# Kernel optimization log

Hardware: AMD Instinct MI355X
Metric: run time of the kernel (lower is better)

Reference implementation:

```python
import jax, jax.numpy as jnp
import numpy as np

D_MODEL = 1024
N_HEADS = 16
D_K = D_MODEL // N_HEADS
B, T = 4, 2048


def setup_inputs() -> dict:
    key = jax.random.key(0)
    ks = jax.random.split(key, 12)
    s = 1.0 / np.sqrt(D_MODEL)
    inp = {
        "query": jax.random.normal(ks[0], (B, T, D_MODEL), dtype=jnp.float32),
        "key": jax.random.normal(ks[1], (B, T, D_MODEL), dtype=jnp.float32),
        "value": jax.random.normal(ks[2], (B, T, D_MODEL), dtype=jnp.float32),
        # causal mask, broadcastable over batch and heads
        "mask": jnp.tril(jnp.ones((T, T), dtype=bool))[None, None, :, :],
        "W_q": jax.random.uniform(ks[3], (D_MODEL, D_MODEL), jnp.float32, -s, s),
        "b_q": jnp.zeros((D_MODEL,), jnp.float32),
        "W_k": jax.random.uniform(ks[4], (D_MODEL, D_MODEL), jnp.float32, -s, s),
        "b_k": jnp.zeros((D_MODEL,), jnp.float32),
        "W_v": jax.random.uniform(ks[5], (D_MODEL, D_MODEL), jnp.float32, -s, s),
        "b_v": jnp.zeros((D_MODEL,), jnp.float32),
        "W_o": jax.random.uniform(ks[6], (D_MODEL, D_MODEL), jnp.float32, -s, s),
        "b_o": jnp.zeros((D_MODEL,), jnp.float32),
    }
    return inp


def _split_heads(x):
    b, t, _ = x.shape
    return x.reshape(b, t, N_HEADS, D_K).transpose(0, 2, 1, 3)  # [B,H,T,Dk]


def reference(query, key, value, mask, W_q, b_q, W_k, b_k, W_v, b_v, W_o, b_o):
    q = _split_heads(query @ W_q.T + b_q)
    k = _split_heads(key @ W_k.T + b_k)
    v = _split_heads(value @ W_v.T + b_v)
    scale = 1.0 / jnp.sqrt(jnp.asarray(D_K, q.dtype))
    scores = jnp.einsum("bhqd,bhkd->bhqk", q, k) * scale  # [B,H,Tq,Tk]
    scores = jnp.where(mask, scores, jnp.asarray(-jnp.inf, scores.dtype))
    attn = jax.nn.softmax(scores, axis=-1)
    out = jnp.einsum("bhqk,bhkd->bhqd", attn, v)
    out = out.transpose(0, 2, 1, 3).reshape(query.shape[0], query.shape[1], D_MODEL)
    return out @ W_o.T + b_o
```

## Files before the change

### kernel.cpp

```cpp
#include <hip/hip_runtime.h>
#include <stdint.h>
#include <stddef.h>


typedef __attribute__((ext_vector_type(4))) float f32x4;
typedef __attribute__((ext_vector_type(8))) _Float16 f16x8;
typedef __attribute__((ext_vector_type(4))) _Float16 f16x4;

#define DEV __device__ __forceinline__

constexpr int BATCH = 4, SEQ = 2048, NH = 16, DK = 64, DM = 1024;
constexpr int MROWS = BATCH * SEQ;
constexpr float QSCALE = 0.125f * 1.4426950408889634f;

DEV void async16(const void* g, void* l) {
  __builtin_amdgcn_global_load_lds(
      (const __attribute__((address_space(1))) unsigned int*)g,
      (__attribute__((address_space(3))) unsigned int*)l, 16, 0, 0);
}

__global__ void cvt_w_kernel(const float* __restrict__ w0, const float* __restrict__ w1,
                             const float* __restrict__ w2, const float* __restrict__ w3,
                             _Float16* __restrict__ o0, _Float16* __restrict__ o1,
                             _Float16* __restrict__ o2, _Float16* __restrict__ o3) {
  size_t i = (size_t)blockIdx.x * blockDim.x + threadIdx.x;
  const float* ws[4] = {w0, w1, w2, w3};
  _Float16* os[4] = {o0, o1, o2, o3};
#pragma unroll
  for (int m = 0; m < 4; m++) {
    f32x4 x = *(const f32x4*)(ws[m] + i * 4);
    f16x4 h;
#pragma unroll
    for (int j = 0; j < 4; j++) h[j] = (_Float16)x[j];
    *(f16x4*)(os[m] + i * 4) = h;
  }
}

__global__ void cvt_act_kernel(const float* __restrict__ a0, const float* __restrict__ a1,
                               const float* __restrict__ a2, _Float16* __restrict__ o0,
                               _Float16* __restrict__ o1, _Float16* __restrict__ o2) {
  size_t i = (size_t)blockIdx.x * blockDim.x + threadIdx.x;
  const float* as[3] = {a0, a1, a2};
  _Float16* os[3] = {o0, o1, o2};
#pragma unroll
  for (int m = 0; m < 3; m++) {
    f32x4 x = *(const f32x4*)(as[m] + i * 4);
    f16x4 h;
#pragma unroll
    for (int j = 0; j < 4; j++) h[j] = (_Float16)x[j];
    *(f16x4*)(os[m] + i * 4) = h;
  }
}

struct QKVPtrs {
  const float* a32[3];
  const _Float16* a16[3];
  const _Float16* w[3];
  const float* bias[3];
  _Float16* out[3];
};

DEV void stage_g16(const _Float16* __restrict__ src, int k0, _Float16* dst, int tid) {
  const int wave = tid >> 6;
#pragma unroll
  for (int it = 0; it < 4; it++) {
    int idx = it * 256 + tid;
    int row = idx >> 3, seg = idx & 7;
    async16(src + (size_t)row * DM + k0 + ((seg ^ (row & 7)) << 3),
            (char*)dst + (size_t)(it * 256 + wave * 64) * 16);
  }
}

DEV void stage_f32(const float* __restrict__ src, int k0, _Float16* dst, int tid) {
#pragma unroll
  for (int it = 0; it < 4; it++) {
    int idx = it * 256 + tid;
    int row = idx >> 3, seg = idx & 7;
    const float* g = src + (size_t)row * DM + k0 + seg * 8;
    f32x4 x0 = *(const f32x4*)g;
    f32x4 x1 = *(const f32x4*)(g + 4);
    f16x8 h;
#pragma unroll
    for (int j = 0; j < 4; j++) { h[j] = (_Float16)x0[j]; h[4 + j] = (_Float16)x1[j]; }
    *(f16x8*)&dst[row * 64 + ((seg ^ (row & 7)) << 3)] = h;
  }
}

template <bool AH>
__global__ __launch_bounds__(256) void gemm_qkv_kernel(QKVPtrs P) {
  constexpr int K = DM;
  __shared__ __align__(16) _Float16 smem[4 * 128 * 64];
  const int z = blockIdx.z;
  const _Float16* Bw = P.w[z];
  const int tid = threadIdx.x;
  const int wave = tid >> 6, lane = tid & 63;
  const int quad = lane >> 4, l16 = lane & 15;
  const int wm = wave >> 1, wn = wave & 1;
  const int m0 = blockIdx.x * 128, n0 = blockIdx.y * 128;
  const float scale = (z == 0) ? QSCALE : 1.0f;

  const _Float16* Bg = Bw + (size_t)n0 * K;
  const _Float16* Ag16 = AH ? P.a16[z] + (size_t)m0 * K : nullptr;
  const float* Ag32 = AH ? nullptr : P.a32[z] + (size_t)m0 * K;

  const f32x4 zero4 = {0.f, 0.f, 0.f, 0.f};
  f32x4 acc[4][4];
#pragma unroll
  for (int mt = 0; mt < 4; mt++)
#pragma unroll
    for (int nt = 0; nt < 4; nt++) acc[mt][nt] = zero4;

  float bv[4];
#pragma unroll
  for (int nt = 0; nt < 4; nt++) bv[nt] = P.bias[z][n0 + wn * 64 + nt * 16 + l16];

  stage_g16(Bg, 0, smem + 8192, tid);
  if (AH) stage_g16(Ag16, 0, smem, tid);
  else    stage_f32(Ag32, 0, smem, tid);
  __syncthreads();

  for (int kt = 0; kt < K / 64; kt++) {
    const int boff = (kt & 1) ? 16384 : 0;
    const _Float16* Asc = smem + boff;
    const _Float16* Bsc = smem + 8192 + boff;
    if (kt + 1 < K / 64) {
      const int k0 = (kt + 1) * 64;
      const int poff = boff ^ 16384;
      stage_g16(Bg, k0, smem + 8192 + poff, tid);
      if (AH) stage_g16(Ag16, k0, smem + poff, tid);
      else    stage_f32(Ag32, k0, smem + poff, tid);
    }
    __builtin_amdgcn_s_setprio(1);
#pragma unroll
    for (int ks = 0; ks < 2; ks++) {
      f16x8 af[4], bfr[4];
#pragma unroll
      for (int mt = 0; mt < 4; mt++) {
        int r = wm * 64 + mt * 16 + l16;
        af[mt] = *(const f16x8*)&Asc[r * 64 + (((ks * 4 + quad) ^ (r & 7)) << 3)];
      }
#pragma unroll
      for (int nt = 0; nt < 4; nt++) {
        int r = wn * 64 + nt * 16 + l16;
        bfr[nt] = *(const f16x8*)&Bsc[r * 64 + (((ks * 4 + quad) ^ (r & 7)) << 3)];
      }
#pragma unroll
      for (int mt = 0; mt < 4; mt++)
#pragma unroll
        for (int nt = 0; nt < 4; nt++)
          acc[mt][nt] = __builtin_amdgcn_mfma_f32_16x16x32_f16(af[mt], bfr[nt], acc[mt][nt], 0, 0, 0);
    }
    __builtin_amdgcn_s_setprio(0);
    __syncthreads();
  }

  _Float16* Ct = smem;
  const int b = m0 >> 11, tbase = m0 & (SEQ - 1);
  if (z < 2) {
#pragma unroll
    for (int mt = 0; mt < 4; mt++)
#pragma unroll
      for (int nt = 0; nt < 4; nt++)
#pragma unroll
        for (int i = 0; i < 4; i++)
          Ct[(wm * 64 + mt * 16 + quad * 4 + i) * 144 + wn * 64 + nt * 16 + l16] =
              (_Float16)((acc[mt][nt][i] + bv[nt]) * scale);
  } else {
#pragma unroll
    for (int mt = 0; mt < 4; mt++)
#pragma unroll
      for (int nt = 0; nt < 4; nt++)
#pragma unroll
        for (int i = 0; i < 4; i++)
          Ct[(wn * 64 + nt * 16 + l16) * 144 + wm * 64 + mt * 16 + quad * 4 + i] =
              (_Float16)(acc[mt][nt][i] + bv[nt]);
  }
  __syncthreads();
  _Float16* out = P.out[z];
  if (z < 2) {
    const int row = tid >> 1, coff = (tid & 1) * 32;
#pragma unroll
    for (int hh = 0; hh < 2; hh++) {
      int h = (n0 >> 6) + hh;
      size_t gb = ((size_t)(b * NH + h) * SEQ + tbase) * 64 + (size_t)tid * 32;
#pragma unroll
      for (int k2 = 0; k2 < 4; k2++)
        *(f16x8*)&out[gb + k2 * 8] =
            *(const f16x8*)&Ct[row * 144 + hh * 64 + coff + k2 * 8];
    }
  } else {
#pragma unroll
    for (int k2 = 0; k2 < 8; k2++) {
      int c = k2 * 256 + tid;
      int n = c >> 4, s2 = c & 15;
      int h = (n0 + n) >> 6, d = (n0 + n) & (DK - 1);
      size_t gb = ((size_t)(b * NH + h) * DK + d) * SEQ + tbase + s2 * 8;
      *(f16x8*)&out[gb] = *(const f16x8*)&Ct[n * 144 + s2 * 8];
    }
  }
}

__global__ __launch_bounds__(256) void gemm_out_kernel(
    const _Float16* __restrict__ Ah, const _Float16* __restrict__ Bw,
    const float* __restrict__ bias, float* __restrict__ Cp) {
  constexpr int K = DM;
  __shared__ __align__(16) _Float16 smem[4 * 128 * 64];
  const int tid = threadIdx.x;
  const int wave = tid >> 6, lane = tid & 63;
  const int quad = lane >> 4, l16 = lane & 15;
  const int wm = wave >> 1, wn = wave & 1;
  const int m0 = blockIdx.x * 128, n0 = blockIdx.y * 128;

  const _Float16* Bg = Bw + (size_t)n0 * K;
  const _Float16* Ag = Ah + (size_t)m0 * K;

  const f32x4 zero4 = {0.f, 0.f, 0.f, 0.f};
  f32x4 acc[4][4];
#pragma unroll
  for (int mt = 0; mt < 4; mt++)
#pragma unroll
    for (int nt = 0; nt < 4; nt++) acc[mt][nt] = zero4;

  float bv[4];
#pragma unroll
  for (int nt = 0; nt < 4; nt++) bv[nt] = bias[n0 + wn * 64 + nt * 16 + l16];

  stage_g16(Bg, 0, smem + 8192, tid);
  stage_g16(Ag, 0, smem, tid);
  __syncthreads();

  for (int kt = 0; kt < K / 64; kt++) {
    const int boff = (kt & 1) ? 16384 : 0;
    const _Float16* Asc = smem + boff;
    const _Float16* Bsc = smem + 8192 + boff;
    if (kt + 1 < K / 64) {
      const int k0 = (kt + 1) * 64;
      const int poff = boff ^ 16384;
      stage_g16(Bg, k0, smem + 8192 + poff, tid);
      stage_g16(Ag, k0, smem + poff, tid);
    }
    __builtin_amdgcn_s_setprio(1);
#pragma unroll
    for (int ks = 0; ks < 2; ks++) {
      f16x8 af[4], bfr[4];
#pragma unroll
      for (int mt = 0; mt < 4; mt++) {
        int r = wm * 64 + mt * 16 + l16;
        af[mt] = *(const f16x8*)&Asc[r * 64 + (((ks * 4 + quad) ^ (r & 7)) << 3)];
      }
#pragma unroll
      for (int nt = 0; nt < 4; nt++) {
        int r = wn * 64 + nt * 16 + l16;
        bfr[nt] = *(const f16x8*)&Bsc[r * 64 + (((ks * 4 + quad) ^ (r & 7)) << 3)];
      }
#pragma unroll
      for (int mt = 0; mt < 4; mt++)
#pragma unroll
        for (int nt = 0; nt < 4; nt++)
          acc[mt][nt] = __builtin_amdgcn_mfma_f32_16x16x32_f16(af[mt], bfr[nt], acc[mt][nt], 0, 0, 0);
    }
    __builtin_amdgcn_s_setprio(0);
    __syncthreads();
  }
#pragma unroll
  for (int mt = 0; mt < 4; mt++)
#pragma unroll
    for (int nt = 0; nt < 4; nt++)
#pragma unroll
      for (int i = 0; i < 4; i++) {
        int m = m0 + wm * 64 + mt * 16 + quad * 4 + i;
        int n = n0 + wn * 64 + nt * 16 + l16;
        Cp[(size_t)m * DM + n] = acc[mt][nt][i] + bv[nt];
      }
}

__global__ __launch_bounds__(256, 2) void attn_kernel(
    const _Float16* __restrict__ Q, const _Float16* __restrict__ Kt,
    const _Float16* __restrict__ V, _Float16* __restrict__ O) {
  __shared__ __align__(16) _Float16 Ks[128 * 72];
  __shared__ __align__(16) _Float16 Vs[64 * 136];
  const int tid = threadIdx.x;
  const int wave = tid >> 6, lane = tid & 63, quad = lane >> 4, l16 = lane & 15;
  const int bh = blockIdx.y;
  const size_t base = (size_t)bh * SEQ * DK;
  const int b = bh >> 4, h = bh & 15;
  const f32x4 zero4 = {0.f, 0.f, 0.f, 0.f};

  for (int p = 0; p < 2; p++) {
    const int qt = (p == 0) ? (int)blockIdx.x : 15 - (int)blockIdx.x;
    const int t0 = qt * 128;

    f16x8 qf[2][2];
#pragma unroll
    for (int mt = 0; mt < 2; mt++)
#pragma unroll
      for (int ks = 0; ks < 2; ks++)
        qf[mt][ks] = *(const f16x8*)(Q + base + (size_t)(t0 + wave * 32 + mt * 16 + l16) * DK +
                                     ks * 32 + quad * 8);

    f32x4 oacc[2][4];
#pragma unroll
    for (int mt = 0; mt < 2; mt++)
#pragma unroll
      for (int nt = 0; nt < 4; nt++) oacc[mt][nt] = zero4;
    float mrow[2] = {-1e30f, -1e30f}, lrow[2] = {0.f, 0.f};

    for (int j = 0; j <= qt; j++) {
#pragma unroll
      for (int it = 0; it < 4; it++) {
        int c = it * 256 + tid;
        int row = c >> 3, off = (c & 7) * 8;
        *(f16x8*)&Ks[row * 72 + off] =
            *(const f16x8*)(Kt + base + (size_t)(j * 128 + row) * 64 + off);
      }
#pragma unroll
      for (int it = 0; it < 4; it++) {
        int c = it * 256 + tid;
        int d = c >> 4, off = (c & 15) * 8;
        *(f16x8*)&Vs[d * 136 + off] =
            *(const f16x8*)(V + base + ((size_t)d << 11) + j * 128 + off);
      }
      __syncthreads();

      f32x4 s[2][8];
#pragma unroll
      for (int nt = 0; nt < 8; nt++) {
        f16x8 kf0 = *(const f16x8*)&Ks[(nt * 16 + l16) * 72 + quad * 8];
        f16x8 kf1 = *(const f16x8*)&Ks[(nt * 16 + l16) * 72 + 32 + quad * 8];
#pragma unroll
        for (int mt = 0; mt < 2; mt++) {
          f32x4 zz = zero4;
          zz = __builtin_amdgcn_mfma_f32_16x16x32_f16(kf0, qf[mt][0], zz, 0, 0, 0);
          zz = __builtin_amdgcn_mfma_f32_16x16x32_f16(kf1, qf[mt][1], zz, 0, 0, 0);
          s[mt][nt] = zz;
        }
      }
      if (j == qt) {
#pragma unroll
        for (int mt = 0; mt < 2; mt++) {
          int qloc = wave * 32 + mt * 16 + l16;
#pragma unroll
          for (int nt = 0; nt < 8; nt++)
#pragma unroll
            for (int i = 0; i < 4; i++)
              if (nt * 16 + quad * 4 + i > qloc) s[mt][nt][i] = -1e30f;
        }
      }
#pragma unroll
      for (int mt = 0; mt < 2; mt++) {
        float mx = mrow[mt];
#pragma unroll
        for (int nt = 0; nt < 8; nt++)
#pragma unroll
          for (int i = 0; i < 4; i++) mx = fmaxf(mx, s[mt][nt][i]);
        mx = fmaxf(mx, __shfl_xor(mx, 16));
        mx = fmaxf(mx, __shfl_xor(mx, 32));
        float alpha = __builtin_exp2f(mrow[mt] - mx);
        mrow[mt] = mx;
        float rs = 0.f;
#pragma unroll
        for (int nt = 0; nt < 8; nt++)
#pragma unroll
          for (int i = 0; i < 4; i++) {
            float pv = __builtin_exp2f(s[mt][nt][i] - mx);
            s[mt][nt][i] = pv;
            rs += pv;
          }
        rs += __shfl_xor(rs, 16);
        rs += __shfl_xor(rs, 32);
        lrow[mt] = lrow[mt] * alpha + rs;
#pragma unroll
        for (int i = 0; i < 4; i++) {
          float ab = __shfl(alpha, quad * 4 + i);
#pragma unroll
          for (int nt = 0; nt < 4; nt++) oacc[mt][nt][i] *= ab;
        }
      }
#pragma unroll
      for (int jj = 0; jj < 8; jj++) {
        f16x4 pf[2];
#pragma unroll
        for (int mt = 0; mt < 2; mt++) {
          f16x4 t;
#pragma unroll
          for (int i = 0; i < 4; i++) t[i] = (_Float16)s[mt][jj][i];
          pf[mt] = t;
        }
#pragma unroll
        for (int nt = 0; nt < 4; nt++) {
          f16x4 vb = *(const f16x4*)&Vs[(nt * 16 + l16) * 136 + jj * 16 + quad * 4];
#pragma unroll
          for (int mt = 0; mt < 2; mt++)
            oacc[mt][nt] = __builtin_amdgcn_mfma_f32_16x16x16f16(pf[mt], vb, oacc[mt][nt], 0, 0, 0);
        }
      }
      __syncthreads();
    }
#pragma unroll
    for (int mt = 0; mt < 2; mt++) {
      float linv = 1.0f / lrow[mt];
#pragma unroll
      for (int i = 0; i < 4; i++) {
        float lb = __shfl(linv, quad * 4 + i);
        int t = t0 + wave * 32 + mt * 16 + quad * 4 + i;
#pragma unroll
        for (int nt = 0; nt < 4; nt++) {
          int d = nt * 16 + l16;
          O[((size_t)(b * SEQ + t) << 10) + h * 64 + d] = (_Float16)(oacc[mt][nt][i] * lb);
        }
      }
    }
  }
}

extern "C" void kernel_launch(void* const* d_in, const int* in_sizes, int n_in,
                              void* d_out, int out_size, void* d_ws, size_t ws_size,
                              hipStream_t stream) {
  const float* query = (const float*)d_in[0];
  const float* key_  = (const float*)d_in[1];
  const float* value = (const float*)d_in[2];
  const float* W_q = (const float*)d_in[4];
  const float* b_q = (const float*)d_in[5];
  const float* W_k = (const float*)d_in[6];
  const float* b_k = (const float*)d_in[7];
  const float* W_v = (const float*)d_in[8];
  const float* b_v = (const float*)d_in[9];
  const float* W_o = (const float*)d_in[10];
  const float* b_o = (const float*)d_in[11];

  constexpr size_t WEL = (size_t)DM * DM;
  constexpr size_t MEL = (size_t)MROWS * DM;
  _Float16* ws = (_Float16*)d_ws;
  _Float16* wq = ws;
  _Float16* wk = wq + WEL;
  _Float16* wv = wk + WEL;
  _Float16* wo = wv + WEL;

  const bool big = ws_size >= (size_t)(4 * WEL + 6 * MEL) * sizeof(_Float16);

  QKVPtrs P;
  P.a32[0] = query; P.a32[1] = key_; P.a32[2] = value;
  P.w[0] = wq; P.w[1] = wk; P.w[2] = wv;
  P.bias[0] = b_q; P.bias[1] = b_k; P.bias[2] = b_v;

  cvt_w_kernel<<<dim3((unsigned)(WEL / 4 / 256)), 256, 0, stream>>>(
      W_q, W_k, W_v, W_o, wq, wk, wv, wo);

  _Float16 *qb, *kb, *vb, *ab;
  if (big) {
    _Float16* qh = wo + WEL;
    _Float16* kh = qh + MEL;
    _Float16* vh = kh + MEL;
    qb = vh + MEL; kb = qb + MEL; vb = kb + MEL;
    ab = qh;
    P.a16[0] = qh; P.a16[1] = kh; P.a16[2] = vh;
    P.out[0] = qb; P.out[1] = kb; P.out[2] = vb;
    cvt_act_kernel<<<dim3((unsigned)(MEL / 4 / 256)), 256, 0, stream>>>(
        query, key_, value, qh, kh, vh);
    gemm_qkv_kernel<true><<<dim3(MROWS / 128, DM / 128, 3), 256, 0, stream>>>(P);
  } else {
    qb = wo + WEL; kb = qb + MEL; vb = kb + MEL; ab = vb + MEL;
    P.a16[0] = P.a16[1] = P.a16[2] = nullptr;
    P.out[0] = qb; P.out[1] = kb; P.out[2] = vb;
    gemm_qkv_kernel<false><<<dim3(MROWS / 128, DM / 128, 3), 256, 0, stream>>>(P);
  }

  attn_kernel<<<dim3(8, BATCH * NH), 256, 0, stream>>>(qb, kb, vb, ab);

  gemm_out_kernel<<<dim3(MROWS / 128, DM / 128), 256, 0, stream>>>(ab, wo, b_o, (float*)d_out);
}
```

Before: 329.7 us.

## Double-buffer K/V tiles in attention with async global-to-LDS loads and XOR swizzle

Replaces the synchronous register-staged K/V tile loads in the attention loop with async global_load_lds into two LDS buffers, prefetching tile j+1 while tile j is computed. Padded LDS rows are replaced by an XOR-swizzled layout to avoid bank conflicts without padding, and MFMA sections are wrapped in s_setprio raises. The aim is to hide global load latency behind compute. LDS usage roughly doubles, which may affect the two-blocks-per-CU occupancy. A single __syncthreads per iteration is relied on for ordering between the async writes and the reads.

New measurement: 335.4 us. Within noise of the previous version (+1.7%).

```diff
diff --git a/kernel.cpp b/kernel.cpp
--- a/kernel.cpp
+++ b/kernel.cpp
@@ -277,8 +277,8 @@
 __global__ __launch_bounds__(256, 2) void attn_kernel(
     const _Float16* __restrict__ Q, const _Float16* __restrict__ Kt,
     const _Float16* __restrict__ V, _Float16* __restrict__ O) {
-  __shared__ __align__(16) _Float16 Ks[128 * 72];
-  __shared__ __align__(16) _Float16 Vs[64 * 136];
+  __shared__ __align__(16) _Float16 Ks[2 * 128 * 64];
+  __shared__ __align__(16) _Float16 Vs[2 * 64 * 128];
   const int tid = threadIdx.x;
   const int wave = tid >> 6, lane = tid & 63, quad = lane >> 4, l16 = lane & 15;
   const int bh = blockIdx.y;
@@ -286,6 +286,13 @@
   const int b = bh >> 4, h = bh & 15;
   const f32x4 zero4 = {0.f, 0.f, 0.f, 0.f};
 
+  int koffs[2], voffs[8];
+#pragma unroll
+  for (int ks = 0; ks < 2; ks++) koffs[ks] = ((ks * 4 + quad) ^ (l16 & 7)) << 3;
+#pragma unroll
+  for (int jj = 0; jj < 8; jj++)
+    voffs[jj] = (((jj * 2 + (quad >> 1)) ^ l16) << 3) + (quad & 1) * 4;
+
   for (int p = 0; p < 2; p++) {
     const int qt = (p == 0) ? (int)blockIdx.x : 15 - (int)blockIdx.x;
     const int t0 = qt * 128;
@@ -305,28 +312,56 @@
       for (int nt = 0; nt < 4; nt++) oacc[mt][nt] = zero4;
     float mrow[2] = {-1e30f, -1e30f}, lrow[2] = {0.f, 0.f};
 
+    {
+      const int wbase = wave * 64;
+#pragma unroll
+      for (int it = 0; it < 4; it++) {
+        int idx = it * 256 + tid;
+        int row = idx >> 3, seg = idx & 7;
+        async16(Kt + base + (size_t)row * 64 + ((seg ^ (row & 7)) << 3),
+                (char*)Ks + (size_t)(it * 256 + wbase) * 16);
+      }
+#pragma unroll
+      for (int it = 0; it < 4; it++) {
+        int idx = it * 256 + tid;
+        int d = idx >> 4, g = idx & 15;
+        async16(V + base + ((size_t)d << 11) + ((g ^ (d & 15)) << 3),
+                (char*)Vs + (size_t)(it * 256 + wbase) * 16);
+      }
+    }
+    __syncthreads();
+
     for (int j = 0; j <= qt; j++) {
-#pragma unroll
-      for (int it = 0; it < 4; it++) {
-        int c = it * 256 + tid;
-        int row = c >> 3, off = (c & 7) * 8;
-        *(f16x8*)&Ks[row * 72 + off] =
-            *(const f16x8*)(Kt + base + (size_t)(j * 128 + row) * 64 + off);
-      }
-#pragma unroll
-      for (int it = 0; it < 4; it++) {
-        int c = it * 256 + tid;
-        int d = c >> 4, off = (c & 15) * 8;
-        *(f16x8*)&Vs[d * 136 + off] =
-            *(const f16x8*)(V + base + ((size_t)d << 11) + j * 128 + off);
-      }
-      __syncthreads();
+      const int koff = (j & 1) ? 8192 : 0;
+      const _Float16* Kb = Ks + koff;
+      const _Float16* Vb = Vs + koff;
+      if (j < qt) {
+        const int poff = koff ^ 8192;
+        const int wbase = wave * 64;
+        const int jn = (j + 1) * 128;
+#pragma unroll
+        for (int it = 0; it < 4; it++) {
+          int idx = it * 256 + tid;
+          int row = idx >> 3, seg = idx & 7;
+          async16(Kt + base + (size_t)(jn + row) * 64 + ((seg ^ (row & 7)) << 3),
+                  (char*)(Ks + poff) + (size_t)(it * 256 + wbase) * 16);
+        }
+#pragma unroll
+        for (int it = 0; it < 4; it++) {
+          int idx = it * 256 + tid;
+          int d = idx >> 4, g = idx & 15;
+          async16(V + base + ((size_t)d << 11) + jn + ((g ^ (d & 15)) << 3),
+                  (char*)(Vs + poff) + (size_t)(it * 256 + wbase) * 16);
+        }
+      }
 
       f32x4 s[2][8];
+      __builtin_amdgcn_s_setprio(1);
 #pragma unroll
       for (int nt = 0; nt < 8; nt++) {
-        f16x8 kf0 = *(const f16x8*)&Ks[(nt * 16 + l16) * 72 + quad * 8];
-        f16x8 kf1 = *(const f16x8*)&Ks[(nt * 16 + l16) * 72 + 32 + quad * 8];
+        int rb = (nt * 16 + l16) * 64;
+        f16x8 kf0 = *(const f16x8*)&Kb[rb + koffs[0]];
+        f16x8 kf1 = *(const f16x8*)&Kb[rb + koffs[1]];
 #pragma unroll
         for (int mt = 0; mt < 2; mt++) {
           f32x4 zz = zero4;
@@ -335,6 +370,7 @@
           s[mt][nt] = zz;
         }
       }
+      __builtin_amdgcn_s_setprio(0);
       if (j == qt) {
 #pragma unroll
         for (int mt = 0; mt < 2; mt++) {
@@ -376,6 +412,7 @@
           for (int nt = 0; nt < 4; nt++) oacc[mt][nt][i] *= ab;
         }
       }
+      __builtin_amdgcn_s_setprio(1);
 #pragma unroll
       for (int jj = 0; jj < 8; jj++) {
         f16x4 pf[2];
@@ -388,12 +425,13 @@
         }
 #pragma unroll
         for (int nt = 0; nt < 4; nt++) {
-          f16x4 vb = *(const f16x4*)&Vs[(nt * 16 + l16) * 136 + jj * 16 + quad * 4];
+          f16x4 vb = *(const f16x4*)&Vb[(nt * 16 + l16) * 128 + voffs[jj]];
 #pragma unroll
           for (int mt = 0; mt < 2; mt++)
             oacc[mt][nt] = __builtin_amdgcn_mfma_f32_16x16x16f16(pf[mt], vb, oacc[mt][nt], 0, 0, 0);
         }
       }
+      __builtin_amdgcn_s_setprio(0);
       __syncthreads();
     }
 #pragma unroll
```

## Double-buffer attention K/V via async LDS loads with swizzle and lazy rescale

Applied to the files above, without the earlier changes.

The attention kernel is restructured. Each block now handles one query tile, with the grid doubled and a rotated tile assignment for load balance. K/V tiles shrink to 64 keys and are double-buffered in LDS using direct global-to-LDS async loads, and XOR swizzling replaces padding to avoid bank conflicts. Online softmax now rescales only when the running max grows by more than a threshold, which skips alpha multiplies, and wave priority is raised around the MFMA sections. Launch bounds rise to 4 blocks per CU, which may pressure registers. The lazy rescale relies on fp16 headroom for P values up to 2^8.

After: 366.4 us. 11.1% more time.

```diff
diff --git a/kernel.cpp b/kernel.cpp
--- a/kernel.cpp
+++ b/kernel.cpp
@@ -274,101 +274,112 @@
       }
 }
 
-__global__ __launch_bounds__(256, 2) void attn_kernel(
+__global__ __launch_bounds__(256, 4) void attn_kernel(
     const _Float16* __restrict__ Q, const _Float16* __restrict__ Kt,
     const _Float16* __restrict__ V, _Float16* __restrict__ O) {
-  __shared__ __align__(16) _Float16 Ks[128 * 72];
-  __shared__ __align__(16) _Float16 Vs[64 * 136];
+  __shared__ __align__(16) _Float16 Ks[2 * 64 * 64];
+  __shared__ __align__(16) _Float16 Vs[2 * 64 * 64];
   const int tid = threadIdx.x;
   const int wave = tid >> 6, lane = tid & 63, quad = lane >> 4, l16 = lane & 15;
   const int bh = blockIdx.y;
   const size_t base = (size_t)bh * SEQ * DK;
   const int b = bh >> 4, h = bh & 15;
+  const int qt = ((int)blockIdx.x + ((int)blockIdx.y >> 2)) & 15;
+  const int t0 = qt * 128;
+  const int nT = 2 * qt + 2;
   const f32x4 zero4 = {0.f, 0.f, 0.f, 0.f};
 
-  for (int p = 0; p < 2; p++) {
-    const int qt = (p == 0) ? (int)blockIdx.x : 15 - (int)blockIdx.x;
-    const int t0 = qt * 128;
-
-    f16x8 qf[2][2];
-#pragma unroll
-    for (int mt = 0; mt < 2; mt++)
-#pragma unroll
-      for (int ks = 0; ks < 2; ks++)
-        qf[mt][ks] = *(const f16x8*)(Q + base + (size_t)(t0 + wave * 32 + mt * 16 + l16) * DK +
-                                     ks * 32 + quad * 8);
-
-    f32x4 oacc[2][4];
-#pragma unroll
-    for (int mt = 0; mt < 2; mt++)
-#pragma unroll
-      for (int nt = 0; nt < 4; nt++) oacc[mt][nt] = zero4;
-    float mrow[2] = {-1e30f, -1e30f}, lrow[2] = {0.f, 0.f};
-
-    for (int j = 0; j <= qt; j++) {
-#pragma unroll
-      for (int it = 0; it < 4; it++) {
-        int c = it * 256 + tid;
-        int row = c >> 3, off = (c & 7) * 8;
-        *(f16x8*)&Ks[row * 72 + off] =
-            *(const f16x8*)(Kt + base + (size_t)(j * 128 + row) * 64 + off);
-      }
-#pragma unroll
-      for (int it = 0; it < 4; it++) {
-        int c = it * 256 + tid;
-        int d = c >> 4, off = (c & 15) * 8;
-        *(f16x8*)&Vs[d * 136 + off] =
-            *(const f16x8*)(V + base + ((size_t)d << 11) + j * 128 + off);
-      }
-      __syncthreads();
-
-      f32x4 s[2][8];
-#pragma unroll
-      for (int nt = 0; nt < 8; nt++) {
-        f16x8 kf0 = *(const f16x8*)&Ks[(nt * 16 + l16) * 72 + quad * 8];
-        f16x8 kf1 = *(const f16x8*)&Ks[(nt * 16 + l16) * 72 + 32 + quad * 8];
-#pragma unroll
-        for (int mt = 0; mt < 2; mt++) {
-          f32x4 zz = zero4;
-          zz = __builtin_amdgcn_mfma_f32_16x16x32_f16(kf0, qf[mt][0], zz, 0, 0, 0);
-          zz = __builtin_amdgcn_mfma_f32_16x16x32_f16(kf1, qf[mt][1], zz, 0, 0, 0);
-          s[mt][nt] = zz;
-        }
-      }
-      if (j == qt) {
-#pragma unroll
-        for (int mt = 0; mt < 2; mt++) {
-          int qloc = wave * 32 + mt * 16 + l16;
-#pragma unroll
-          for (int nt = 0; nt < 8; nt++)
-#pragma unroll
-            for (int i = 0; i < 4; i++)
-              if (nt * 16 + quad * 4 + i > qloc) s[mt][nt][i] = -1e30f;
-        }
-      }
+  int koffs[2], voffs[4];
+#pragma unroll
+  for (int ks = 0; ks < 2; ks++) koffs[ks] = ((ks * 4 + quad) ^ (l16 & 7)) << 3;
+#pragma unroll
+  for (int jj = 0; jj < 4; jj++)
+    voffs[jj] = (((jj * 2 + (quad >> 1)) ^ (l16 & 7)) << 3) + (quad & 1) * 4;
+
+  f16x8 qf[2][2];
+#pragma unroll
+  for (int mt = 0; mt < 2; mt++)
+#pragma unroll
+    for (int ks = 0; ks < 2; ks++)
+      qf[mt][ks] = *(const f16x8*)(Q + base + (size_t)(t0 + wave * 32 + mt * 16 + l16) * DK +
+                                   ks * 32 + quad * 8);
+
+  f32x4 oacc[2][4];
+#pragma unroll
+  for (int mt = 0; mt < 2; mt++)
+#pragma unroll
+    for (int nt = 0; nt < 4; nt++) oacc[mt][nt] = zero4;
+  float mrow[2] = {-1e30f, -1e30f}, lrow[2] = {0.f, 0.f};
+
+  auto stageKV = [&](int j, int off) {
+    const int wbase = wave * 64;
+    const size_t tk0 = (size_t)j * 64;
+#pragma unroll
+    for (int it = 0; it < 2; it++) {
+      int idx = it * 256 + tid;
+      int row = idx >> 3, seg = idx & 7;
+      async16(Kt + base + (tk0 + row) * 64 + ((seg ^ (row & 7)) << 3),
+              (char*)(Ks + off) + (size_t)(it * 256 + wbase) * 16);
+    }
+#pragma unroll
+    for (int it = 0; it < 2; it++) {
+      int idx = it * 256 + tid;
+      int d = idx >> 3, g = idx & 7;
+      async16(V + base + ((size_t)d << 11) + tk0 + ((g ^ (d & 7)) << 3),
+              (char*)(Vs + off) + (size_t)(it * 256 + wbase) * 16);
+    }
+  };
+
+  stageKV(0, 0);
+  __syncthreads();
+
+  for (int j = 0; j < nT; j++) {
+    const int off = (j & 1) * 4096;
+    const _Float16* Kb = Ks + off;
+    const _Float16* Vb = Vs + off;
+    if (j + 1 < nT) stageKV(j + 1, off ^ 4096);
+
+    f32x4 s[2][4];
+    __builtin_amdgcn_s_setprio(1);
+#pragma unroll
+    for (int nt = 0; nt < 4; nt++) {
+      int rb = (nt * 16 + l16) * 64;
+      f16x8 kf0 = *(const f16x8*)&Kb[rb + koffs[0]];
+      f16x8 kf1 = *(const f16x8*)&Kb[rb + koffs[1]];
 #pragma unroll
       for (int mt = 0; mt < 2; mt++) {
-        float mx = mrow[mt];
-#pragma unroll
-        for (int nt = 0; nt < 8; nt++)
-#pragma unroll
-          for (int i = 0; i < 4; i++) mx = fmaxf(mx, s[mt][nt][i]);
-        mx = fmaxf(mx, __shfl_xor(mx, 16));
-        mx = fmaxf(mx, __shfl_xor(mx, 32));
+        f32x4 zz = zero4;
+        zz = __builtin_amdgcn_mfma_f32_16x16x32_f16(kf0, qf[mt][0], zz, 0, 0, 0);
+        zz = __builtin_amdgcn_mfma_f32_16x16x32_f16(kf1, qf[mt][1], zz, 0, 0, 0);
+        s[mt][nt] = zz;
+      }
+    }
+    __builtin_amdgcn_s_setprio(0);
+    if (j >= 2 * qt) {
+#pragma unroll
+      for (int mt = 0; mt < 2; mt++) {
+        int qg = t0 + wave * 32 + mt * 16 + l16;
+#pragma unroll
+        for (int nt = 0; nt < 4; nt++)
+#pragma unroll
+          for (int i = 0; i < 4; i++)
+            if (j * 64 + nt * 16 + quad * 4 + i > qg) s[mt][nt][i] = -1e30f;
+      }
+    }
+#pragma unroll
+    for (int mt = 0; mt < 2; mt++) {
+      float tmax = s[mt][0][0];
+#pragma unroll
+      for (int nt = 0; nt < 4; nt++)
+#pragma unroll
+        for (int i = 0; i < 4; i++) tmax = fmaxf(tmax, s[mt][nt][i]);
+      tmax = fmaxf(tmax, __shfl_xor(tmax, 16));
+      tmax = fmaxf(tmax, __shfl_xor(tmax, 32));
+      if (__any(tmax > mrow[mt] + 8.0f)) {
+        float mx = fmaxf(mrow[mt], tmax);
         float alpha = __builtin_exp2f(mrow[mt] - mx);
         mrow[mt] = mx;
-        float rs = 0.f;
-#pragma unroll
-        for (int nt = 0; nt < 8; nt++)
-#pragma unroll
-          for (int i = 0; i < 4; i++) {
-            float pv = __builtin_exp2f(s[mt][nt][i] - mx);
-            s[mt][nt][i] = pv;
-            rs += pv;
-          }
-        rs += __shfl_xor(rs, 16);
-        rs += __shfl_xor(rs, 32);
-        lrow[mt] = lrow[mt] * alpha + rs;
+        lrow[mt] *= alpha;
 #pragma unroll
         for (int i = 0; i < 4; i++) {
           float ab = __shfl(alpha, quad * 4 + i);
@@ -376,38 +387,53 @@
           for (int nt = 0; nt < 4; nt++) oacc[mt][nt][i] *= ab;
         }
       }
-#pragma unroll
-      for (int jj = 0; jj < 8; jj++) {
-        f16x4 pf[2];
-#pragma unroll
-        for (int mt = 0; mt < 2; mt++) {
-          f16x4 t;
-#pragma unroll
-          for (int i = 0; i < 4; i++) t[i] = (_Float16)s[mt][jj][i];
-          pf[mt] = t;
+      float mx = mrow[mt];
+      float rs = 0.f;
+#pragma unroll
+      for (int nt = 0; nt < 4; nt++)
+#pragma unroll
+        for (int i = 0; i < 4; i++) {
+          float pv = __builtin_exp2f(s[mt][nt][i] - mx);
+          s[mt][nt][i] = pv;
+          rs += pv;
         }
-#pragma unroll
-        for (int nt = 0; nt < 4; nt++) {
-          f16x4 vb = *(const f16x4*)&Vs[(nt * 16 + l16) * 136 + jj * 16 + quad * 4];
-#pragma unroll
-          for (int mt = 0; mt < 2; mt++)
-            oacc[mt][nt] = __builtin_amdgcn_mfma_f32_16x16x16f16(pf[mt], vb, oacc[mt][nt], 0, 0, 0);
-        }
-      }
-      __syncthreads();
-    }
-#pragma unroll
-    for (int mt = 0; mt < 2; mt++) {
-      float linv = 1.0f / lrow[mt];
-#pragma unroll
-      for (int i = 0; i < 4; i++) {
-        float lb = __shfl(linv, quad * 4 + i);
-        int t = t0 + wave * 32 + mt * 16 + quad * 4 + i;
-#pragma unroll
-        for (int nt = 0; nt < 4; nt++) {
-          int d = nt * 16 + l16;
-          O[((size_t)(b * SEQ + t) << 10) + h * 64 + d] = (_Float16)(oacc[mt][nt][i] * lb);
-        }
+      rs += __shfl_xor(rs, 16);
+      rs += __shfl_xor(rs, 32);
+      lrow[mt] += rs;
+    }
+    __builtin_amdgcn_s_setprio(1);
+#pragma unroll
+    for (int jj = 0; jj < 4; jj++) {
+      f16x4 pf[2];
+#pragma unroll
+      for (int mt = 0; mt < 2; mt++) {
+        f16x4 t;
+#pragma unroll
+        for (int i = 0; i < 4; i++) t[i] = (_Float16)s[mt][jj][i];
+        pf[mt] = t;
+      }
+#pragma unroll
+      for (int nt = 0; nt < 4; nt++) {
+        f16x4 vb = *(const f16x4*)&Vb[(nt * 16 + l16) * 64 + voffs[jj]];
+#pragma unroll
+        for (int mt = 0; mt < 2; mt++)
+          oacc[mt][nt] = __builtin_amdgcn_mfma_f32_16x16x16f16(pf[mt], vb, oacc[mt][nt], 0, 0, 0);
+      }
+    }
+    __builtin_amdgcn_s_setprio(0);
+    __syncthreads();
+  }
+#pragma unroll
+  for (int mt = 0; mt < 2; mt++) {
+    float linv = 1.0f / lrow[mt];
+#pragma unroll
+    for (int i = 0; i < 4; i++) {
+      float lb = __shfl(linv, quad * 4 + i);
+      int t = t0 + wave * 32 + mt * 16 + quad * 4 + i;
+#pragma unroll
+      for (int nt = 0; nt < 4; nt++) {
+        int d = nt * 16 + l16;
+        O[((size_t)(b * SEQ + t) << 10) + h * 64 + d] = (_Float16)(oacc[mt][nt][i] * lb);
       }
     }
   }
@@ -465,7 +491,7 @@
     gemm_qkv_kernel<false><<<dim3(MROWS / 128, DM / 128, 3), 256, 0, stream>>>(P);
   }
 
-  attn_kernel<<<dim3(8, BATCH * NH), 256, 0, stream>>>(qb, kb, vb, ab);
+  attn_kernel<<<dim3(16, BATCH * NH), 256, 0, stream>>>(qb, kb, vb, ab);
 
   gemm_out_kernel<<<dim3(MROWS / 128, DM / 128), 256, 0, stream>>>(ab, wo, b_o, (float*)d_out);
 }
```
